# Optimization experiments

Hardware: AMD Instinct MI355X
Metric: run time of the kernel (lower is better)

Reference implementation:

```python
import jax, jax.numpy as jnp
import numpy as np

D_NODE = 256
D_PAIR = 128
C = 32
H = 8
LN_EPS = 1e-5


def layer_norm(x, g, b):
    m = jnp.mean(x, axis=-1, keepdims=True)
    v = jnp.mean(jnp.square(x - m), axis=-1, keepdims=True)
    return (x - m) * jax.lax.rsqrt(v + LN_EPS) * g + b


def self_attention(x, mask, wq, wk, wv, wg, bg, wo, bo=None, bias=None):
    # x: [B, S, R, d], mask: [B, S, R]
    B, S, R, _ = x.shape
    scale = 1.0 / np.sqrt(C)
    q = (jnp.einsum('bsrd,ed->bsre', x, wq) * scale).reshape(B, S, R, H, C)
    k = jnp.einsum('bsrd,ed->bsre', x, wk).reshape(B, S, R, H, C)
    v = jnp.einsum('bsrd,ed->bsre', x, wv).reshape(B, S, R, H, C)
    logits = jnp.einsum('bsqhc,bskhc->bshqk', q, k)
    logits = logits + (1e9 * (mask - 1.0))[:, :, None, None, :]
    if bias is not None:
        logits = logits + bias[:, None]  # [B,1,H,R,R]
    a = jax.nn.softmax(logits, axis=-1)
    o = jnp.einsum('bshqk,bskhc->bsqhc', a, v).reshape(B, S, R, H * C)
    g = jax.nn.sigmoid(jnp.einsum('bsrd,ed->bsre', x, wg) + bg)
    out = jnp.einsum('bsre,de->bsrd', o * g, wo)
    if bo is not None:
        out = out + bo
    return out


def setup_inputs() -> dict:
    key = jax.random.key(0)
    ks = jax.random.split(key, 24)
    B, S, R = 1, 128, 256
    d, dp, hc, dff = D_NODE, D_PAIR, H * C, 4 * D_NODE
    std = 0.02
    inp = {
        'node': jax.random.normal(ks[0], (B, S, R, d), jnp.float32),
        'pair': jax.random.normal(ks[1], (B, R, R, dp), jnp.float32),
        'node_mask': jnp.ones((B, S, R), jnp.float32),
        # row attention (pair-biased)
        'row_ln_m_g': jnp.ones((d,), jnp.float32),
        'row_ln_m_b': jnp.zeros((d,), jnp.float32),
        'row_ln_z_g': jnp.ones((dp,), jnp.float32),
        'row_ln_z_b': jnp.zeros((dp,), jnp.float32),
        'row_b_w': jax.random.normal(ks[2], (H, dp), jnp.float32) / np.sqrt(dp),
        'row_wq': jax.random.normal(ks[3], (hc, d), jnp.float32) * std,
        'row_wk': jax.random.normal(ks[4], (hc, d), jnp.float32) * std,
        'row_wv': jax.random.normal(ks[5], (hc, d), jnp.float32) * std,
        'row_wg': jax.random.normal(ks[6], (hc, d), jnp.float32) * std,
        'row_bg': jnp.ones((hc,), jnp.float32),
        'row_wo': jax.random.normal(ks[7], (d, hc), jnp.float32) * std,
        'row_out_bias': jnp.zeros((d,), jnp.float32),
        # column attention
        'col_ln_g': jnp.ones((d,), jnp.float32),
        'col_ln_b': jnp.zeros((d,), jnp.float32),
        'col_wq': jax.random.normal(ks[8], (hc, d), jnp.float32) * std,
        'col_wk': jax.random.normal(ks[9], (hc, d), jnp.float32) * std,
        'col_wv': jax.random.normal(ks[10], (hc, d), jnp.float32) * std,
        'col_wg': jax.random.normal(ks[11], (hc, d), jnp.float32) * std,
        'col_bg': jnp.ones((hc,), jnp.float32),
        'col_wo': jax.random.normal(ks[12], (d, hc), jnp.float32) * std,
        'col_bo': jnp.zeros((d,), jnp.float32),
        # transition
        'tr_ln_g': jnp.ones((d,), jnp.float32),
        'tr_ln_b': jnp.zeros((d,), jnp.float32),
        'tr_w1': jax.random.normal(ks[13], (dff, d), jnp.float32) * std,
        'tr_b1': jnp.zeros((dff,), jnp.float32),
        'tr_w2': jax.random.normal(ks[14], (d, dff), jnp.float32) * std,
        'tr_b2': jnp.zeros((d,), jnp.float32),
    }
    return inp


def reference(node, pair, node_mask,
              row_ln_m_g, row_ln_m_b, row_ln_z_g, row_ln_z_b, row_b_w,
              row_wq, row_wk, row_wv, row_wg, row_bg, row_wo, row_out_bias,
              col_ln_g, col_ln_b, col_wq, col_wk, col_wv, col_wg, col_bg,
              col_wo, col_bo, tr_ln_g, tr_ln_b, tr_w1, tr_b1, tr_w2, tr_b2):
    # --- MSA row attention with pair bias ---
    M = layer_norm(node, row_ln_m_g, row_ln_m_b)
    Z = layer_norm(pair, row_ln_z_g, row_ln_z_b)
    b = jnp.einsum('bqkd,hd->bhqk', Z, row_b_w)  # pair bias [B,H,R,R]
    attn = self_attention(M, node_mask, row_wq, row_wk, row_wv,
                          row_wg, row_bg, row_wo, bo=None, bias=b)
    # bias_dropout_add in eval mode: residual + attn + fused out bias
    node = node + attn + row_out_bias
    # --- MSA column attention ---
    Mt = jnp.swapaxes(node, 1, 2)            # [B,R,S,d]
    Mn = layer_norm(Mt, col_ln_g, col_ln_b)
    mask_t = jnp.swapaxes(node_mask, 1, 2)   # [B,R,S]
    attn_c = self_attention(Mn, mask_t, col_wq, col_wk, col_wv,
                            col_wg, col_bg, col_wo, bo=col_bo)
    node = node + jnp.swapaxes(attn_c, 1, 2)
    # --- MSA transition ---
    t = layer_norm(node, tr_ln_g, tr_ln_b)
    t = jax.nn.relu(jnp.einsum('bsrd,ed->bsre', t, tr_w1) + tr_b1)
    node = node + (jnp.einsum('bsre,de->bsrd', t, tr_w2) + tr_b2)
    return node
```

## Files before the change

kernel.cpp:

```cpp
#include <hip/hip_runtime.h>
#include <math.h>

#define S 128
#define R 256
#define DMODEL 256
#define H 8
#define CDIM 32
#define HC 256
#define DFF 1024
#define NROWS (S*R)
#define NPAIR (R*R)
#define LN_EPS 1e-5f
#define LOG2E 1.4426950408889634f
#define M32 ((size_t)NROWS * 32)

typedef unsigned short u16;
typedef __attribute__((ext_vector_type(8))) short bf16x8;
typedef __attribute__((ext_vector_type(4))) float f32x4;
typedef __attribute__((ext_vector_type(16))) float f32x16;

__device__ __forceinline__ u16 f2bf(float x) {
  unsigned u = __float_as_uint(x);
  u = (u + 0x7fffu + ((u >> 16) & 1u)) >> 16;
  return (u16)u;
}
__device__ __forceinline__ float bf2f(u16 x) {
  return __uint_as_float(((unsigned)x) << 16);
}
__device__ __forceinline__ unsigned cvt_pk(float a, float b) {
  unsigned r;
  asm("v_cvt_pk_bf16_f32 %0, %1, %2" : "=v"(r) : "v"(a), "v"(b));
  return r;
}
__device__ __forceinline__ void pl32swap(unsigned &a, unsigned &b) {
  asm("v_permlane32_swap_b32 %0, %1" : "+v"(a), "+v"(b));
}
__device__ __forceinline__ bf16x8 mk_frag(unsigned a, unsigned b, unsigned c, unsigned d) {
  uint4 t = make_uint4(a, b, c, d);
  return __builtin_bit_cast(bf16x8, t);
}

__device__ __forceinline__ void gload_lds16(const u16* g, u16* l) {
  __builtin_amdgcn_global_load_lds(
      (const __attribute__((address_space(1))) unsigned int*)g,
      (__attribute__((address_space(3))) unsigned int*)l, 16, 0, 0);
}

struct CvtArgs {
  const float* src[12];
  int off[12];
  int n[12];
  float scale[12];
};

__global__ __launch_bounds__(256) void cvt_w_kernel(CvtArgs a, u16* __restrict__ dst) {
  int sg = blockIdx.y;
  int i = (blockIdx.x * 256 + threadIdx.x) * 4;
  if (i >= a.n[sg]) return;
  float4 v = *(const float4*)(a.src[sg] + i);
  float sc = a.scale[sg];
  uint2 o;
  o.x = cvt_pk(v.x * sc, v.y * sc);
  o.y = cvt_pk(v.z * sc, v.w * sc);
  *(uint2*)(dst + a.off[sg] + i) = o;
}

__global__ __launch_bounds__(256) void ln256_kernel(
    const void* __restrict__ in, u16* __restrict__ out,
    const float* __restrict__ gamma, const float* __restrict__ beta,
    int tmode, int inbf)
{
  int wid = threadIdx.x >> 6, lane = threadIdx.x & 63;
  int m = blockIdx.x * 4 + wid;
  int inrow = m;
  if (tmode) { int r = m >> 7, s = m & 127; inrow = s * R + r; }
  float4 x;
  if (inbf) {
    ushort4 u = *(const ushort4*)((const u16*)in + (size_t)inrow * DMODEL + lane * 4);
    x.x = bf2f(u.x); x.y = bf2f(u.y); x.z = bf2f(u.z); x.w = bf2f(u.w);
  } else {
    x = *(const float4*)((const float*)in + (size_t)inrow * DMODEL + lane * 4);
  }
  float sum = x.x + x.y + x.z + x.w;
  float sq  = x.x*x.x + x.y*x.y + x.z*x.z + x.w*x.w;
  #pragma unroll
  for (int off = 32; off; off >>= 1) {
    sum += __shfl_xor(sum, off);
    sq  += __shfl_xor(sq, off);
  }
  float mean = sum * (1.0f/256.0f);
  float var  = sq  * (1.0f/256.0f) - mean*mean;
  float rstd = rsqrtf(var + LN_EPS);
  float4 g = *(const float4*)(gamma + lane*4);
  float4 b = *(const float4*)(beta  + lane*4);
  uint2 o;
  o.x = cvt_pk((x.x-mean)*rstd*g.x + b.x, (x.y-mean)*rstd*g.y + b.y);
  o.y = cvt_pk((x.z-mean)*rstd*g.z + b.z, (x.w-mean)*rstd*g.w + b.w);
  *(uint2*)(out + (size_t)m * DMODEL + lane*4) = o;
}

__global__ __launch_bounds__(256) void pair_bias_kernel(
    const float* __restrict__ pair, const float* __restrict__ gamma,
    const float* __restrict__ beta, const float* __restrict__ bw,
    u16* __restrict__ bias)
{
  int wid = threadIdx.x >> 6, lane = threadIdx.x & 63;
  int p = blockIdx.x * 4 + wid;
  float2 x = *(const float2*)(pair + (size_t)p * 128 + lane*2);
  float sum = x.x + x.y, sq = x.x*x.x + x.y*x.y;
  #pragma unroll
  for (int off = 32; off; off >>= 1) {
    sum += __shfl_xor(sum, off);
    sq  += __shfl_xor(sq, off);
  }
  float mean = sum * (1.0f/128.0f);
  float rstd = rsqrtf(sq*(1.0f/128.0f) - mean*mean + LN_EPS);
  float z0 = (x.x-mean)*rstd*gamma[lane*2]   + beta[lane*2];
  float z1 = (x.y-mean)*rstd*gamma[lane*2+1] + beta[lane*2+1];
  float a0 = z0*bw[0*128+lane*2] + z1*bw[0*128+lane*2+1];
  float a1 = z0*bw[1*128+lane*2] + z1*bw[1*128+lane*2+1];
  float a2 = z0*bw[2*128+lane*2] + z1*bw[2*128+lane*2+1];
  float a3 = z0*bw[3*128+lane*2] + z1*bw[3*128+lane*2+1];
  float a4 = z0*bw[4*128+lane*2] + z1*bw[4*128+lane*2+1];
  float a5 = z0*bw[5*128+lane*2] + z1*bw[5*128+lane*2+1];
  float a6 = z0*bw[6*128+lane*2] + z1*bw[6*128+lane*2+1];
  float a7 = z0*bw[7*128+lane*2] + z1*bw[7*128+lane*2+1];
  #pragma unroll
  for (int off = 32; off; off >>= 1) {
    a0 += __shfl_xor(a0, off); a1 += __shfl_xor(a1, off);
    a2 += __shfl_xor(a2, off); a3 += __shfl_xor(a3, off);
    a4 += __shfl_xor(a4, off); a5 += __shfl_xor(a5, off);
    a6 += __shfl_xor(a6, off); a7 += __shfl_xor(a7, off);
  }
  float v = a0;
  v = (lane==1)?a1:v; v = (lane==2)?a2:v; v = (lane==3)?a3:v;
  v = (lane==4)?a4:v; v = (lane==5)?a5:v; v = (lane==6)?a6:v; v = (lane==7)?a7:v;
  if (lane < 8) {
    int q = p >> 8, k = p & 255;
    int kt = k >> 5, qt = q >> 5, c31 = q & 31;
    int kk = k & 31;
    int hi2 = (kk >> 2) & 1;
    int j = (kk & 3) | ((kk >> 3) << 2);
    size_t addr = ((((size_t)lane*8 + kt)*8 + qt)*2 + hi2)*512 + (size_t)c31*16 + j;
    bias[addr] = f2bf(v * LOG2E);
  }
}

template<int AM>
__global__ __launch_bounds__(512, 2) void gemm_8ph(
    const u16* __restrict__ A, const u16* __restrict__ W,
    void* __restrict__ Cout, int N, int K,
    int mode, const float* __restrict__ bias, const float* __restrict__ res)
{
  __shared__ u16 lds[2][AM+2][128*32];
  int t = threadIdx.x, lane = t & 63, wv = t >> 6;
  int g16 = (lane >> 4) & 3, l16 = lane & 15;
  int wm = wv >> 2, wn = wv & 3;

  int gx = gridDim.x;
  int nwg = gx * gridDim.y;
  int p = blockIdx.y * gx + blockIdx.x;
  int cpx = nwg >> 3;
  int lg = (p & 7) * cpx + (p >> 3);
  int bn = (lg % gx) * 256;
  int bm = (lg / gx) * (AM * 128);

  int sr = t >> 2;
  int swz8 = ((t & 3) ^ ((sr >> 1) & 3)) << 3;
  int rdch = (g16 ^ ((l16 >> 1) & 3)) << 3;
  int rdoff = l16 * 32 + rdch;
  const int wnh = AM + (wn >> 1);
  const int wnr = (wn & 1) * 2048;

  f32x4 acc[AM*4][4];
  #pragma unroll
  for (int i = 0; i < AM*4; ++i)
    #pragma unroll
    for (int j = 0; j < 4; ++j) acc[i][j] = (f32x4){0.f,0.f,0.f,0.f};

  const int nkt = K >> 5;

#define STAGE(buf_, kc_) do { \
    gload_lds16(A + (size_t)(bm + sr) * K + (kc_) + swz8, &lds[buf_][0][t*8]); \
    if (AM == 2) \
      gload_lds16(A + (size_t)(bm + 128 + sr) * K + (kc_) + swz8, &lds[buf_][1][t*8]); \
    gload_lds16(W + (size_t)(bn + sr) * K + (kc_) + swz8, &lds[buf_][AM][t*8]); \
    gload_lds16(W + (size_t)(bn + 128 + sr) * K + (kc_) + swz8, &lds[buf_][AM+1][t*8]); \
  } while(0)

  STAGE(0, 0);
  for (int kt = 0; kt < nkt; ++kt) {
    if (kt + 1 < nkt) {
      STAGE((kt + 1) & 1, (kt + 1) * 32);
      if (AM == 2) asm volatile("s_waitcnt vmcnt(4)" ::: "memory");
      else         asm volatile("s_waitcnt vmcnt(3)" ::: "memory");
    } else {
      asm volatile("s_waitcnt vmcnt(0)" ::: "memory");
    }
    __builtin_amdgcn_s_barrier();
    int buf = kt & 1;
    const u16* Abase = (AM == 2) ? &lds[buf][wm][0] : &lds[buf][0][wm*2048];
    const u16* Wbase = &lds[buf][wnh][wnr];
    bf16x8 wf[4];
    #pragma unroll
    for (int nf = 0; nf < 4; ++nf)
      wf[nf] = *(const bf16x8*)(Wbase + nf*512 + rdoff);
    __builtin_amdgcn_s_setprio(1);
    #pragma unroll
    for (int mf = 0; mf < AM*4; ++mf) {
      bf16x8 a0 = *(const bf16x8*)(Abase + mf*512 + rdoff);
      #pragma unroll
      for (int nf = 0; nf < 4; ++nf)
        acc[mf][nf] = __builtin_amdgcn_mfma_f32_16x16x32_bf16(wf[nf], a0, acc[mf][nf], 0, 0, 0);
    }
    __builtin_amdgcn_s_setprio(0);
    asm volatile("" ::: "memory");
    __builtin_amdgcn_s_barrier();
  }
#undef STAGE

  const u16* resb = (const u16*)res;
  int rowb = bm + wm*(AM*64) + l16;
  int colb = bn + wn*64 + (g16 << 2);
  #pragma unroll
  for (int mf = 0; mf < AM*4; ++mf) {
    int row = rowb + mf*16;
    #pragma unroll
    for (int nf = 0; nf < 4; ++nf) {
      int col0 = colb + nf*16;
      f32x4 v = acc[mf][nf];
      if (mode == 6) {
        if (col0 >= 768) {
          float4 b4 = *(const float4*)(bias + col0 - 768);
          v[0] = 1.0f/(1.0f+__expf(-(v[0]+b4.x)));
          v[1] = 1.0f/(1.0f+__expf(-(v[1]+b4.y)));
          v[2] = 1.0f/(1.0f+__expf(-(v[2]+b4.z)));
          v[3] = 1.0f/(1.0f+__expf(-(v[3]+b4.w)));
        }
        uint2 o; o.x = cvt_pk(v[0], v[1]); o.y = cvt_pk(v[2], v[3]);
        size_t i2 = (size_t)(col0 >> 5) * M32 + (size_t)row*32 + (col0 & 31);
        *(uint2*)((u16*)Cout + i2) = o;
      } else if (mode == 3) {
        float4 b4 = *(const float4*)(bias + col0);
        uint2 o;
        o.x = cvt_pk(fmaxf(v[0]+b4.x, 0.f), fmaxf(v[1]+b4.y, 0.f));
        o.y = cvt_pk(fmaxf(v[2]+b4.z, 0.f), fmaxf(v[3]+b4.w, 0.f));
        *(uint2*)((u16*)Cout + (size_t)row*N + col0) = o;
      } else if (mode == 4) {
        size_t i2 = (size_t)row*N + col0;
        float4 r4 = *(const float4*)(res + i2);
        float4 b4 = *(const float4*)(bias + col0);
        float4 o = make_float4(v[0]+r4.x+b4.x, v[1]+r4.y+b4.y,
                               v[2]+r4.z+b4.z, v[3]+r4.w+b4.w);
        *(float4*)((float*)Cout + i2) = o;
      } else if (mode == 5) {
        int rr = row >> 7, ss = row & 127;
        size_t i2 = ((size_t)ss*R + rr)*(size_t)N + col0;
        float4 r4 = *(const float4*)(res + i2);
        float4 b4 = *(const float4*)(bias + col0);
        float4 o = make_float4(v[0]+r4.x+b4.x, v[1]+r4.y+b4.y,
                               v[2]+r4.z+b4.z, v[3]+r4.w+b4.w);
        *(float4*)((float*)Cout + i2) = o;
      } else if (mode == 7) {
        size_t i2 = (size_t)row*N + col0;
        float4 r4 = *(const float4*)(res + i2);
        float4 b4 = *(const float4*)(bias + col0);
        uint2 o;
        o.x = cvt_pk(v[0]+r4.x+b4.x, v[1]+r4.y+b4.y);
        o.y = cvt_pk(v[2]+r4.z+b4.z, v[3]+r4.w+b4.w);
        *(uint2*)((u16*)Cout + i2) = o;
      } else if (mode == 8) {
        int rr = row >> 7, ss = row & 127;
        size_t i2 = ((size_t)ss*R + rr)*(size_t)N + col0;
        ushort4 r4 = *(const ushort4*)(resb + i2);
        float4 b4 = *(const float4*)(bias + col0);
        uint2 o;
        o.x = cvt_pk(v[0]+bf2f(r4.x)+b4.x, v[1]+bf2f(r4.y)+b4.y);
        o.y = cvt_pk(v[2]+bf2f(r4.z)+b4.z, v[3]+bf2f(r4.w)+b4.w);
        *(uint2*)((u16*)Cout + i2) = o;
      } else if (mode == 9) {
        size_t i2 = (size_t)row*N + col0;
        ushort4 r4 = *(const ushort4*)(resb + i2);
        float4 b4 = *(const float4*)(bias + col0);
        float4 o = make_float4(v[0]+bf2f(r4.x)+b4.x, v[1]+bf2f(r4.y)+b4.y,
                               v[2]+bf2f(r4.z)+b4.z, v[3]+bf2f(r4.w)+b4.w);
        *(float4*)((float*)Cout + i2) = o;
      } else if (mode == 2) {
        float4 b4 = *(const float4*)(bias + col0);
        uint2 o;
        o.x = cvt_pk(1.0f/(1.0f+__expf(-(v[0]+b4.x))),
                     1.0f/(1.0f+__expf(-(v[1]+b4.y))));
        o.y = cvt_pk(1.0f/(1.0f+__expf(-(v[2]+b4.z))),
                     1.0f/(1.0f+__expf(-(v[3]+b4.w))));
        *(uint2*)((u16*)Cout + (size_t)row*N + col0) = o;
      } else {
        uint2 o; o.x = cvt_pk(v[0], v[1]); o.y = cvt_pk(v[2], v[3]);
        *(uint2*)((u16*)Cout + (size_t)row*N + col0) = o;
      }
    }
  }
}

template<bool RM>
__device__ __forceinline__ void softmax_pack(
    const f32x16 &sac, const float* __restrict__ lmbp,
    bf16x8 bf0, bf16x8 bf1, int kb, int hi,
    float &lsum, bf16x8 &pf0, bf16x8 &pf1)
{
  float p[16];
  #pragma unroll
  for (int rq = 0; rq < 4; ++rq) {
    int k0 = kb + 8*rq + 4*hi;
    float4 lm4 = *(const float4*)&lmbp[k0];
    float b0 = lm4.x, b1 = lm4.y, b2 = lm4.z, b3 = lm4.w;
    if (RM) {
      if (rq < 2) {
        b0 += bf2f((u16)bf0[4*rq+0]); b1 += bf2f((u16)bf0[4*rq+1]);
        b2 += bf2f((u16)bf0[4*rq+2]); b3 += bf2f((u16)bf0[4*rq+3]);
      } else {
        b0 += bf2f((u16)bf1[4*rq-8+0]); b1 += bf2f((u16)bf1[4*rq-8+1]);
        b2 += bf2f((u16)bf1[4*rq-8+2]); b3 += bf2f((u16)bf1[4*rq-8+3]);
      }
    }
    p[4*rq+0] = exp2f(sac[4*rq+0] + b0);
    p[4*rq+1] = exp2f(sac[4*rq+1] + b1);
    p[4*rq+2] = exp2f(sac[4*rq+2] + b2);
    p[4*rq+3] = exp2f(sac[4*rq+3] + b3);
    lsum += (p[4*rq+0] + p[4*rq+1]) + (p[4*rq+2] + p[4*rq+3]);
  }
  unsigned u0 = cvt_pk(p[0],  p[1]),  u1 = cvt_pk(p[2],  p[3]);
  unsigned u2 = cvt_pk(p[4],  p[5]),  u3 = cvt_pk(p[6],  p[7]);
  unsigned u4 = cvt_pk(p[8],  p[9]),  u5 = cvt_pk(p[10], p[11]);
  unsigned u6 = cvt_pk(p[12], p[13]), u7 = cvt_pk(p[14], p[15]);
  pl32swap(u0, u2); pl32swap(u1, u3);
  pl32swap(u4, u6); pl32swap(u5, u7);
  pf0 = mk_frag(u0, u1, u2, u3);
  pf1 = mk_frag(u4, u5, u6, u7);
}

template<int NKEY, int HPB, bool ROWMODE>
__global__ __launch_bounds__(512, 2) void attn_mfma(
    const u16* __restrict__ QKVG, const u16* __restrict__ biasF,
    const float* __restrict__ mask, u16* __restrict__ og)
{
  __shared__ __align__(16) u16 Vt[HPB][32][NKEY + 8];
  __shared__ float lmb[NKEY];
  constexpr int NKV = NKEY / 32;
  constexpr int WPH = 8 / HPB;
  int b = blockIdx.y;
  int t = threadIdx.x, lane = t & 63, w = t >> 6;
  int c31 = lane & 31, hi = lane >> 5;
  int lh = w / WPH, wtile = w % WPH;
  int hh = blockIdx.x * HPB + lh;

  size_t rbase = (size_t)b * NKEY * 32;
  const u16* Qp = QKVG + (size_t)hh * M32 + rbase;
  const u16* Kp = QKVG + (size_t)(8 + hh) * M32 + rbase;
  const u16* Gp = QKVG + (size_t)(24 + hh) * M32 + rbase;

  for (int i = t; i < HPB*NKEY*4; i += 512) {
    int c0 = (i & 3) * 8;
    int key = (i >> 2) & (NKEY - 1);
    int sh = (i >> 2) / NKEY;
    const u16* Vs = QKVG + (size_t)(16 + blockIdx.x*HPB + sh) * M32 + rbase;
    bf16x8 v8 = *(const bf16x8*)(Vs + (size_t)key*32 + c0);
    #pragma unroll
    for (int j = 0; j < 8; ++j) Vt[sh][c0+j][key] = (u16)v8[j];
  }
  for (int i = t; i < NKEY; i += 512)
    lmb[i] = 1.4426950e9f * ((ROWMODE ? mask[b*R + i] : mask[i*R + b]) - 1.0f);
  __syncthreads();

  int qA = wtile*64 + c31, qB = qA + 32;
  int qtA = wtile*2, qtB = wtile*2 + 1;
  bf16x8 qfA0 = *(const bf16x8*)(Qp + (size_t)qA*32 + hi*8);
  bf16x8 qfA1 = *(const bf16x8*)(Qp + (size_t)qA*32 + 16 + hi*8);
  bf16x8 qfB0 = *(const bf16x8*)(Qp + (size_t)qB*32 + hi*8);
  bf16x8 qfB1 = *(const bf16x8*)(Qp + (size_t)qB*32 + 16 + hi*8);

  f32x16 oA = (f32x16)(0.0f), oB = (f32x16)(0.0f);
  float lsA = 0.f, lsB = 0.f;

#define LOADK(d0_, d1_, g_) do { \
    const u16* kr_ = Kp + ((size_t)((g_)*32) + c31)*32 + hi*8; \
    d0_ = *(const bf16x8*)kr_; d1_ = *(const bf16x8*)(kr_ + 16); \
  } while(0)

#define GROUP_BODY(g_, k0_, k1_) do { \
    int kb_ = (g_) * 32; \
    bf16x8 bA0{}, bA1{}, bB0{}, bB1{}; \
    if (ROWMODE) { \
      const u16* bpA_ = biasF + ((((size_t)hh*8 + (g_))*8 + qtA)*2 + hi)*512 + (size_t)c31*16; \
      bA0 = *(const bf16x8*)bpA_; bA1 = *(const bf16x8*)(bpA_ + 8); \
    } \
    __builtin_amdgcn_s_setprio(1); \
    f32x16 sacA_ = __builtin_amdgcn_mfma_f32_32x32x16_bf16(k0_, qfA0, (f32x16)(0.0f), 0, 0, 0); \
    sacA_ = __builtin_amdgcn_mfma_f32_32x32x16_bf16(k1_, qfA1, sacA_, 0, 0, 0); \
    __builtin_amdgcn_s_setprio(0); \
    bf16x8 va0_ = *(const bf16x8*)&Vt[lh][c31][kb_ + hi*8]; \
    bf16x8 va1_ = *(const bf16x8*)&Vt[lh][c31][kb_ + 16 + hi*8]; \
    bf16x8 pf0_, pf1_; \
    softmax_pack<ROWMODE>(sacA_, lmb, bA0, bA1, kb_, hi, lsA, pf0_, pf1_); \
    __builtin_amdgcn_s_setprio(1); \
    oA = __builtin_amdgcn_mfma_f32_32x32x16_bf16(va0_, pf0_, oA, 0, 0, 0); \
    oA = __builtin_amdgcn_mfma_f32_32x32x16_bf16(va1_, pf1_, oA, 0, 0, 0); \
    __builtin_amdgcn_s_setprio(0); \
    if (ROWMODE) { \
      const u16* bpB_ = biasF + ((((size_t)hh*8 + (g_))*8 + qtB)*2 + hi)*512 + (size_t)c31*16; \
      bB0 = *(const bf16x8*)bpB_; bB1 = *(const bf16x8*)(bpB_ + 8); \
    } \
    __builtin_amdgcn_s_setprio(1); \
    f32x16 sacB_ = __builtin_amdgcn_mfma_f32_32x32x16_bf16(k0_, qfB0, (f32x16)(0.0f), 0, 0, 0); \
    sacB_ = __builtin_amdgcn_mfma_f32_32x32x16_bf16(k1_, qfB1, sacB_, 0, 0, 0); \
    __builtin_amdgcn_s_setprio(0); \
    softmax_pack<ROWMODE>(sacB_, lmb, bB0, bB1, kb_, hi, lsB, pf0_, pf1_); \
    __builtin_amdgcn_s_setprio(1); \
    oB = __builtin_amdgcn_mfma_f32_32x32x16_bf16(va0_, pf0_, oB, 0, 0, 0); \
    oB = __builtin_amdgcn_mfma_f32_32x32x16_bf16(va1_, pf1_, oB, 0, 0, 0); \
    __builtin_amdgcn_s_setprio(0); \
  } while(0)

  bf16x8 ke0{}, ke1{}, ko0{}, ko1{};
  LOADK(ke0, ke1, 0);
  LOADK(ko0, ko1, 1);
  for (int g = 0; g < NKV; g += 2) {
    bf16x8 c0 = ke0, c1 = ke1;
    if (g + 2 < NKV) LOADK(ke0, ke1, g + 2);
    GROUP_BODY(g, c0, c1);
    bf16x8 d0 = ko0, d1 = ko1;
    if (g + 3 < NKV) LOADK(ko0, ko1, g + 3);
    GROUP_BODY(g + 1, d0, d1);
  }
#undef GROUP_BODY
#undef LOADK

  lsA += __shfl_xor(lsA, 32);
  lsB += __shfl_xor(lsB, 32);
  float invA = 1.0f / lsA, invB = 1.0f / lsB;

  size_t baseO = (size_t)b * NKEY * 256 + (size_t)hh * 32;
  #pragma unroll
  for (int tile = 0; tile < 2; ++tile) {
    int q = (tile == 0) ? qA : qB;
    float inv = (tile == 0) ? invA : invB;
    const f32x16 &oo = (tile == 0) ? oA : oB;
    u16* op = og + baseO + (size_t)q * 256;
    const u16* gp = Gp + (size_t)q * 32;
    #pragma unroll
    for (int rq = 0; rq < 4; ++rq) {
      int c0 = 8*rq + 4*hi;
      ushort4 g4 = *(const ushort4*)(gp + c0);
      float f0 = oo[4*rq+0] * inv * bf2f(g4.x);
      float f1 = oo[4*rq+1] * inv * bf2f(g4.y);
      float f2 = oo[4*rq+2] * inv * bf2f(g4.z);
      float f3 = oo[4*rq+3] * inv * bf2f(g4.w);
      uint2 o2; o2.x = cvt_pk(f0, f1); o2.y = cvt_pk(f2, f3);
      *(uint2*)(op + c0) = o2;
    }
  }
}

extern "C" void kernel_launch(void* const* d_in, const int* in_sizes, int n_in,
                              void* d_out, int out_size, void* d_ws, size_t ws_size,
                              hipStream_t stream)
{
  const float* node         = (const float*)d_in[0];
  const float* pair         = (const float*)d_in[1];
  const float* node_mask    = (const float*)d_in[2];
  const float* row_ln_m_g   = (const float*)d_in[3];
  const float* row_ln_m_b   = (const float*)d_in[4];
  const float* row_ln_z_g   = (const float*)d_in[5];
  const float* row_ln_z_b   = (const float*)d_in[6];
  const float* row_b_w      = (const float*)d_in[7];
  const float* row_wq       = (const float*)d_in[8];
  const float* row_wk       = (const float*)d_in[9];
  const float* row_wv       = (const float*)d_in[10];
  const float* row_wg       = (const float*)d_in[11];
  const float* row_bg       = (const float*)d_in[12];
  const float* row_wo       = (const float*)d_in[13];
  const float* row_out_bias = (const float*)d_in[14];
  const float* col_ln_g     = (const float*)d_in[15];
  const float* col_ln_b     = (const float*)d_in[16];
  const float* col_wq       = (const float*)d_in[17];
  const float* col_wk       = (const float*)d_in[18];
  const float* col_wv       = (const float*)d_in[19];
  const float* col_wg       = (const float*)d_in[20];
  const float* col_bg       = (const float*)d_in[21];
  const float* col_wo       = (const float*)d_in[22];
  const float* col_bo       = (const float*)d_in[23];
  const float* tr_ln_g      = (const float*)d_in[24];
  const float* tr_ln_b      = (const float*)d_in[25];
  const float* tr_w1        = (const float*)d_in[26];
  const float* tr_b1        = (const float*)d_in[27];
  const float* tr_w2        = (const float*)d_in[28];
  const float* tr_b2        = (const float*)d_in[29];

  float* out = (float*)d_out;
  char* ws8 = (char*)d_ws;
  const size_t MB = 1ull << 20;
  u16*   A     = (u16*)(ws8);
  u16*   QKVG  = (u16*)(ws8 + 16*MB);
  u16*   Ob    = (u16*)(ws8 + 80*MB);
  u16*   DbF   = (u16*)(ws8 + 96*MB);
  u16*   N1    = (u16*)(ws8 + 100*MB);
  u16*   N2    = (u16*)(ws8 + 116*MB);
  u16*   Wb    = (u16*)(ws8 + 132*MB);
  u16*   T1    = QKVG;

  const float qs = 0.17677669529663687f;

  u16* Wrqkvg = Wb + 0;
  u16* Wro    = Wb + 262144;
  u16* Wcqkvg = Wb + 327680;
  u16* Wco    = Wb + 589824;
  u16* W1w    = Wb + 655360;
  u16* W2w    = Wb + 917504;

  CvtArgs ca;
  const float* srcs[12] = {row_wq,row_wk,row_wv,row_wg,row_wo,
                           col_wq,col_wk,col_wv,col_wg,col_wo,tr_w1,tr_w2};
  int offs[12] = {0,65536,131072,196608,262144,327680,393216,458752,524288,589824,655360,917504};
  int ns[12]   = {65536,65536,65536,65536,65536,65536,65536,65536,65536,65536,262144,262144};
  for (int i = 0; i < 12; ++i) {
    ca.src[i] = srcs[i]; ca.off[i] = offs[i]; ca.n[i] = ns[i];
    ca.scale[i] = (i == 0 || i == 5) ? qs * LOG2E : 1.0f;
  }
  cvt_w_kernel<<<dim3(256,12), 256, 0, stream>>>(ca, Wb);

  dim3 gq(4, 128);
  dim3 go(1, 256);

  ln256_kernel<<<8192, 256, 0, stream>>>(node, A, row_ln_m_g, row_ln_m_b, 0, 0);
  pair_bias_kernel<<<16384, 256, 0, stream>>>(pair, row_ln_z_g, row_ln_z_b, row_b_w, DbF);
  gemm_8ph<2><<<gq, 512, 0, stream>>>(A, Wrqkvg, QKVG, 1024, 256, 6, row_bg, nullptr);
  attn_mfma<256,2,true><<<dim3(4,128), 512, 0, stream>>>(QKVG, DbF, node_mask, Ob);
  gemm_8ph<1><<<go, 512, 0, stream>>>(Ob, Wro, N1, 256, 256, 7, row_out_bias, node);

  ln256_kernel<<<8192, 256, 0, stream>>>(N1, A, col_ln_g, col_ln_b, 1, 1);
  gemm_8ph<2><<<gq, 512, 0, stream>>>(A, Wcqkvg, QKVG, 1024, 256, 6, col_bg, nullptr);
  attn_mfma<128,4,false><<<dim3(2,256), 512, 0, stream>>>(QKVG, nullptr, node_mask, Ob);
  gemm_8ph<1><<<go, 512, 0, stream>>>(Ob, Wco, N2, 256, 256, 8, col_bo, (const float*)N1);

  ln256_kernel<<<8192, 256, 0, stream>>>(N2, A, tr_ln_g, tr_ln_b, 0, 1);
  gemm_8ph<2><<<gq, 512, 0, stream>>>(A, W1w, T1, 1024, 256, 3, tr_b1, nullptr);
  gemm_8ph<1><<<go, 512, 0, stream>>>(T1, W2w, out, 256, 1024, 9, tr_b2, (const float*)N2);
}
```

Measured before the change: 352.1 us.

## Add single-shot K=256 GEMM kernel with full-K LDS staging and smaller tiles

Adds a new GEMM kernel for all K=256 projections. It loads the whole 128x256 A and W tiles into LDS in one pass, with no double-buffered K loop, and uses 128x128 output tiles over a larger grid. The old templated kernel is specialised into a K=1024 variant used only for the second transition GEMM, and the epilogue moves into a shared helper. The change removes per-K-step barriers and pipeline overhead and raises the block count, but allows only one block per CU because of 128KB of LDS, and it reloads inputs more often because the tiles are smaller.

Result: no change. 349.9 us (-0.6%).

```diff
diff --git a/kernel.cpp b/kernel.cpp
--- a/kernel.cpp
+++ b/kernel.cpp
@@ -146,13 +146,140 @@
   }
 }
 
-template<int AM>
-__global__ __launch_bounds__(512, 2) void gemm_8ph(
+__device__ __forceinline__ void epi_store(
+    int mode, void* __restrict__ Cout, int N,
+    const float* __restrict__ bias, const float* __restrict__ res,
+    int row, int col0, f32x4 v)
+{
+  const u16* resb = (const u16*)res;
+  if (mode == 6) {
+    if (col0 >= 768) {
+      float4 b4 = *(const float4*)(bias + col0 - 768);
+      v[0] = 1.0f/(1.0f+__expf(-(v[0]+b4.x)));
+      v[1] = 1.0f/(1.0f+__expf(-(v[1]+b4.y)));
+      v[2] = 1.0f/(1.0f+__expf(-(v[2]+b4.z)));
+      v[3] = 1.0f/(1.0f+__expf(-(v[3]+b4.w)));
+    }
+    uint2 o; o.x = cvt_pk(v[0], v[1]); o.y = cvt_pk(v[2], v[3]);
+    size_t i2 = (size_t)(col0 >> 5) * M32 + (size_t)row*32 + (col0 & 31);
+    *(uint2*)((u16*)Cout + i2) = o;
+  } else if (mode == 3) {
+    float4 b4 = *(const float4*)(bias + col0);
+    uint2 o;
+    o.x = cvt_pk(fmaxf(v[0]+b4.x, 0.f), fmaxf(v[1]+b4.y, 0.f));
+    o.y = cvt_pk(fmaxf(v[2]+b4.z, 0.f), fmaxf(v[3]+b4.w, 0.f));
+    *(uint2*)((u16*)Cout + (size_t)row*N + col0) = o;
+  } else if (mode == 7) {
+    size_t i2 = (size_t)row*N + col0;
+    float4 r4 = *(const float4*)(res + i2);
+    float4 b4 = *(const float4*)(bias + col0);
+    uint2 o;
+    o.x = cvt_pk(v[0]+r4.x+b4.x, v[1]+r4.y+b4.y);
+    o.y = cvt_pk(v[2]+r4.z+b4.z, v[3]+r4.w+b4.w);
+    *(uint2*)((u16*)Cout + i2) = o;
+  } else if (mode == 8) {
+    int rr = row >> 7, ss = row & 127;
+    size_t i2 = ((size_t)ss*R + rr)*(size_t)N + col0;
+    ushort4 r4 = *(const ushort4*)(resb + i2);
+    float4 b4 = *(const float4*)(bias + col0);
+    uint2 o;
+    o.x = cvt_pk(v[0]+bf2f(r4.x)+b4.x, v[1]+bf2f(r4.y)+b4.y);
+    o.y = cvt_pk(v[2]+bf2f(r4.z)+b4.z, v[3]+bf2f(r4.w)+b4.w);
+    *(uint2*)((u16*)Cout + i2) = o;
+  } else if (mode == 9) {
+    size_t i2 = (size_t)row*N + col0;
+    ushort4 r4 = *(const ushort4*)(resb + i2);
+    float4 b4 = *(const float4*)(bias + col0);
+    float4 o = make_float4(v[0]+bf2f(r4.x)+b4.x, v[1]+bf2f(r4.y)+b4.y,
+                           v[2]+bf2f(r4.z)+b4.z, v[3]+bf2f(r4.w)+b4.w);
+    *(float4*)((float*)Cout + i2) = o;
+  } else {
+    uint2 o; o.x = cvt_pk(v[0], v[1]); o.y = cvt_pk(v[2], v[3]);
+    *(uint2*)((u16*)Cout + (size_t)row*N + col0) = o;
+  }
+}
+
+__global__ __launch_bounds__(512, 1) void gemm_flat(
+    const u16* __restrict__ A, const u16* __restrict__ W,
+    void* __restrict__ Cout, int N,
+    int mode, const float* __restrict__ bias, const float* __restrict__ res)
+{
+  __shared__ u16 As[128*256];
+  __shared__ u16 Ws[128*256];
+  int t = threadIdx.x, lane = t & 63;
+  int wv = t >> 6;
+  int g16 = (lane >> 4) & 3, l16 = lane & 15;
+  int wm = wv >> 1, wn = wv & 1;
+
+  int gx = gridDim.x;
+  int nwg = gx * gridDim.y;
+  int p = blockIdx.y * gx + blockIdx.x;
+  int cpx = nwg >> 3;
+  int lg = (p & 7) * cpx + (p >> 3);
+  int bn = (lg % gx) * 128;
+  int bm = (lg / gx) * 128;
+
+  int srow = t >> 5;
+  int dc = t & 31;
+  int sc = (dc & 24) | ((dc & 7) ^ (srow & 7));
+  const u16* Ag = A + (size_t)(bm + srow) * 256 + sc * 8;
+  const u16* Wg = W + (size_t)(bn + srow) * 256 + sc * 8;
+  #pragma unroll
+  for (int i = 0; i < 8; ++i)
+    gload_lds16(Ag + (size_t)i * 16 * 256, &As[i*4096 + t*8]);
+  #pragma unroll
+  for (int i = 0; i < 8; ++i)
+    gload_lds16(Wg + (size_t)i * 16 * 256, &Ws[i*4096 + t*8]);
+  asm volatile("s_waitcnt vmcnt(0)" ::: "memory");
+  __builtin_amdgcn_s_barrier();
+
+  f32x4 acc[2][4];
+  #pragma unroll
+  for (int i = 0; i < 2; ++i)
+    #pragma unroll
+    for (int j = 0; j < 4; ++j) acc[i][j] = (f32x4){0.f,0.f,0.f,0.f};
+
+  int swz8 = l16 & 7;
+  const u16* Abase = As + (size_t)(wm*32 + l16) * 256;
+  const u16* Wbase = Ws + (size_t)(wn*64 + l16) * 256;
+
+  #pragma unroll
+  for (int ks = 0; ks < 8; ++ks) {
+    int c0 = ks * 4 + g16;
+    int rdc = (c0 & 24) | ((c0 & 7) ^ swz8);
+    int off = rdc * 8;
+    bf16x8 wf[4];
+    #pragma unroll
+    for (int nf = 0; nf < 4; ++nf)
+      wf[nf] = *(const bf16x8*)(Wbase + nf*16*256 + off);
+    bf16x8 a0 = *(const bf16x8*)(Abase + off);
+    bf16x8 a1 = *(const bf16x8*)(Abase + 16*256 + off);
+    __builtin_amdgcn_s_setprio(1);
+    #pragma unroll
+    for (int nf = 0; nf < 4; ++nf) {
+      acc[0][nf] = __builtin_amdgcn_mfma_f32_16x16x32_bf16(wf[nf], a0, acc[0][nf], 0, 0, 0);
+      acc[1][nf] = __builtin_amdgcn_mfma_f32_16x16x32_bf16(wf[nf], a1, acc[1][nf], 0, 0, 0);
+    }
+    __builtin_amdgcn_s_setprio(0);
+  }
+
+  int rowb = bm + wm*32 + l16;
+  int colb = bn + wn*64 + (g16 << 2);
+  #pragma unroll
+  for (int mf = 0; mf < 2; ++mf) {
+    int row = rowb + mf*16;
+    #pragma unroll
+    for (int nf = 0; nf < 4; ++nf)
+      epi_store(mode, Cout, N, bias, res, row, colb + nf*16, acc[mf][nf]);
+  }
+}
+
+__global__ __launch_bounds__(512, 2) void gemm_k1024(
     const u16* __restrict__ A, const u16* __restrict__ W,
     void* __restrict__ Cout, int N, int K,
     int mode, const float* __restrict__ bias, const float* __restrict__ res)
 {
-  __shared__ u16 lds[2][AM+2][128*32];
+  __shared__ u16 lds[2][3][128*32];
   int t = threadIdx.x, lane = t & 63, wv = t >> 6;
   int g16 = (lane >> 4) & 3, l16 = lane & 15;
   int wm = wv >> 2, wn = wv & 3;
@@ -163,18 +290,18 @@
   int cpx = nwg >> 3;
   int lg = (p & 7) * cpx + (p >> 3);
   int bn = (lg % gx) * 256;
-  int bm = (lg / gx) * (AM * 128);
+  int bm = (lg / gx) * 128;
 
   int sr = t >> 2;
   int swz8 = ((t & 3) ^ ((sr >> 1) & 3)) << 3;
   int rdch = (g16 ^ ((l16 >> 1) & 3)) << 3;
   int rdoff = l16 * 32 + rdch;
-  const int wnh = AM + (wn >> 1);
+  const int wnh = 1 + (wn >> 1);
   const int wnr = (wn & 1) * 2048;
 
-  f32x4 acc[AM*4][4];
-  #pragma unroll
-  for (int i = 0; i < AM*4; ++i)
+  f32x4 acc[4][4];
+  #pragma unroll
+  for (int i = 0; i < 4; ++i)
     #pragma unroll
     for (int j = 0; j < 4; ++j) acc[i][j] = (f32x4){0.f,0.f,0.f,0.f};
 
@@ -182,24 +309,21 @@
 
 #define STAGE(buf_, kc_) do { \
     gload_lds16(A + (size_t)(bm + sr) * K + (kc_) + swz8, &lds[buf_][0][t*8]); \
-    if (AM == 2) \
-      gload_lds16(A + (size_t)(bm + 128 + sr) * K + (kc_) + swz8, &lds[buf_][1][t*8]); \
-    gload_lds16(W + (size_t)(bn + sr) * K + (kc_) + swz8, &lds[buf_][AM][t*8]); \
-    gload_lds16(W + (size_t)(bn + 128 + sr) * K + (kc_) + swz8, &lds[buf_][AM+1][t*8]); \
+    gload_lds16(W + (size_t)(bn + sr) * K + (kc_) + swz8, &lds[buf_][1][t*8]); \
+    gload_lds16(W + (size_t)(bn + 128 + sr) * K + (kc_) + swz8, &lds[buf_][2][t*8]); \
   } while(0)
 
   STAGE(0, 0);
   for (int kt = 0; kt < nkt; ++kt) {
     if (kt + 1 < nkt) {
       STAGE((kt + 1) & 1, (kt + 1) * 32);
-      if (AM == 2) asm volatile("s_waitcnt vmcnt(4)" ::: "memory");
-      else         asm volatile("s_waitcnt vmcnt(3)" ::: "memory");
+      asm volatile("s_waitcnt vmcnt(3)" ::: "memory");
     } else {
       asm volatile("s_waitcnt vmcnt(0)" ::: "memory");
     }
     __builtin_amdgcn_s_barrier();
     int buf = kt & 1;
-    const u16* Abase = (AM == 2) ? &lds[buf][wm][0] : &lds[buf][0][wm*2048];
+    const u16* Abase = &lds[buf][0][wm*2048];
     const u16* Wbase = &lds[buf][wnh][wnr];
     bf16x8 wf[4];
     #pragma unroll
@@ -207,7 +331,7 @@
       wf[nf] = *(const bf16x8*)(Wbase + nf*512 + rdoff);
     __builtin_amdgcn_s_setprio(1);
     #pragma unroll
-    for (int mf = 0; mf < AM*4; ++mf) {
+    for (int mf = 0; mf < 4; ++mf) {
       bf16x8 a0 = *(const bf16x8*)(Abase + mf*512 + rdoff);
       #pragma unroll
       for (int nf = 0; nf < 4; ++nf)
@@ -219,85 +343,14 @@
   }
 #undef STAGE
 
-  const u16* resb = (const u16*)res;
-  int rowb = bm + wm*(AM*64) + l16;
+  int rowb = bm + wm*64 + l16;
   int colb = bn + wn*64 + (g16 << 2);
   #pragma unroll
-  for (int mf = 0; mf < AM*4; ++mf) {
+  for (int mf = 0; mf < 4; ++mf) {
     int row = rowb + mf*16;
     #pragma unroll
-    for (int nf = 0; nf < 4; ++nf) {
-      int col0 = colb + nf*16;
-      f32x4 v = acc[mf][nf];
-      if (mode == 6) {
-        if (col0 >= 768) {
-          float4 b4 = *(const float4*)(bias + col0 - 768);
-          v[0] = 1.0f/(1.0f+__expf(-(v[0]+b4.x)));
-          v[1] = 1.0f/(1.0f+__expf(-(v[1]+b4.y)));
-          v[2] = 1.0f/(1.0f+__expf(-(v[2]+b4.z)));
-          v[3] = 1.0f/(1.0f+__expf(-(v[3]+b4.w)));
-        }
-        uint2 o; o.x = cvt_pk(v[0], v[1]); o.y = cvt_pk(v[2], v[3]);
-        size_t i2 = (size_t)(col0 >> 5) * M32 + (size_t)row*32 + (col0 & 31);
-        *(uint2*)((u16*)Cout + i2) = o;
-      } else if (mode == 3) {
-        float4 b4 = *(const float4*)(bias + col0);
-        uint2 o;
-        o.x = cvt_pk(fmaxf(v[0]+b4.x, 0.f), fmaxf(v[1]+b4.y, 0.f));
-        o.y = cvt_pk(fmaxf(v[2]+b4.z, 0.f), fmaxf(v[3]+b4.w, 0.f));
-        *(uint2*)((u16*)Cout + (size_t)row*N + col0) = o;
-      } else if (mode == 4) {
-        size_t i2 = (size_t)row*N + col0;
-        float4 r4 = *(const float4*)(res + i2);
-        float4 b4 = *(const float4*)(bias + col0);
-        float4 o = make_float4(v[0]+r4.x+b4.x, v[1]+r4.y+b4.y,
-                               v[2]+r4.z+b4.z, v[3]+r4.w+b4.w);
-        *(float4*)((float*)Cout + i2) = o;
-      } else if (mode == 5) {
-        int rr = row >> 7, ss = row & 127;
-        size_t i2 = ((size_t)ss*R + rr)*(size_t)N + col0;
-        float4 r4 = *(const float4*)(res + i2);
-        float4 b4 = *(const float4*)(bias + col0);
-        float4 o = make_float4(v[0]+r4.x+b4.x, v[1]+r4.y+b4.y,
-                               v[2]+r4.z+b4.z, v[3]+r4.w+b4.w);
-        *(float4*)((float*)Cout + i2) = o;
-      } else if (mode == 7) {
-        size_t i2 = (size_t)row*N + col0;
-        float4 r4 = *(const float4*)(res + i2);
-        float4 b4 = *(const float4*)(bias + col0);
-        uint2 o;
-        o.x = cvt_pk(v[0]+r4.x+b4.x, v[1]+r4.y+b4.y);
-        o.y = cvt_pk(v[2]+r4.z+b4.z, v[3]+r4.w+b4.w);
-        *(uint2*)((u16*)Cout + i2) = o;
-      } else if (mode == 8) {
-        int rr = row >> 7, ss = row & 127;
-        size_t i2 = ((size_t)ss*R + rr)*(size_t)N + col0;
-        ushort4 r4 = *(const ushort4*)(resb + i2);
-        float4 b4 = *(const float4*)(bias + col0);
-        uint2 o;
-        o.x = cvt_pk(v[0]+bf2f(r4.x)+b4.x, v[1]+bf2f(r4.y)+b4.y);
-        o.y = cvt_pk(v[2]+bf2f(r4.z)+b4.z, v[3]+bf2f(r4.w)+b4.w);
-        *(uint2*)((u16*)Cout + i2) = o;
-      } else if (mode == 9) {
-        size_t i2 = (size_t)row*N + col0;
-        ushort4 r4 = *(const ushort4*)(resb + i2);
-        float4 b4 = *(const float4*)(bias + col0);
-        float4 o = make_float4(v[0]+bf2f(r4.x)+b4.x, v[1]+bf2f(r4.y)+b4.y,
-                               v[2]+bf2f(r4.z)+b4.z, v[3]+bf2f(r4.w)+b4.w);
-        *(float4*)((float*)Cout + i2) = o;
-      } else if (mode == 2) {
-        float4 b4 = *(const float4*)(bias + col0);
-        uint2 o;
-        o.x = cvt_pk(1.0f/(1.0f+__expf(-(v[0]+b4.x))),
-                     1.0f/(1.0f+__expf(-(v[1]+b4.y))));
-        o.y = cvt_pk(1.0f/(1.0f+__expf(-(v[2]+b4.z))),
-                     1.0f/(1.0f+__expf(-(v[3]+b4.w))));
-        *(uint2*)((u16*)Cout + (size_t)row*N + col0) = o;
-      } else {
-        uint2 o; o.x = cvt_pk(v[0], v[1]); o.y = cvt_pk(v[2], v[3]);
-        *(uint2*)((u16*)Cout + (size_t)row*N + col0) = o;
-      }
-    }
+    for (int nf = 0; nf < 4; ++nf)
+      epi_store(mode, Cout, N, bias, res, row, colb + nf*16, acc[mf][nf]);
   }
 }
 
@@ -527,21 +580,22 @@
   }
   cvt_w_kernel<<<dim3(256,12), 256, 0, stream>>>(ca, Wb);
 
-  dim3 gq(4, 128);
-  dim3 go(1, 256);
+  dim3 gf1024(8, 256);
+  dim3 gf256(2, 256);
+  dim3 gw2(1, 256);
 
   ln256_kernel<<<8192, 256, 0, stream>>>(node, A, row_ln_m_g, row_ln_m_b, 0, 0);
   pair_bias_kernel<<<16384, 256, 0, stream>>>(pair, row_ln_z_g, row_ln_z_b, row_b_w, DbF);
-  gemm_8ph<2><<<gq, 512, 0, stream>>>(A, Wrqkvg, QKVG, 1024, 256, 6, row_bg, nullptr);
+  gemm_flat<<<gf1024, 512, 0, stream>>>(A, Wrqkvg, QKVG, 1024, 6, row_bg, nullptr);
   attn_mfma<256,2,true><<<dim3(4,128), 512, 0, stream>>>(QKVG, DbF, node_mask, Ob);
-  gemm_8ph<1><<<go, 512, 0, stream>>>(Ob, Wro, N1, 256, 256, 7, row_out_bias, node);
+  gemm_flat<<<gf256, 512, 0, stream>>>(Ob, Wro, N1, 256, 7, row_out_bias, node);
 
   ln256_kernel<<<8192, 256, 0, stream>>>(N1, A, col_ln_g, col_ln_b, 1, 1);
-  gemm_8ph<2><<<gq, 512, 0, stream>>>(A, Wcqkvg, QKVG, 1024, 256, 6, col_bg, nullptr);
+  gemm_flat<<<gf1024, 512, 0, stream>>>(A, Wcqkvg, QKVG, 1024, 6, col_bg, nullptr);
   attn_mfma<128,4,false><<<dim3(2,256), 512, 0, stream>>>(QKVG, nullptr, node_mask, Ob);
-  gemm_8ph<1><<<go, 512, 0, stream>>>(Ob, Wco, N2, 256, 256, 8, col_bo, (const float*)N1);
+  gemm_flat<<<gf256, 512, 0, stream>>>(Ob, Wco, N2, 256, 8, col_bo, (const float*)N1);
 
   ln256_kernel<<<8192, 256, 0, stream>>>(N2, A, tr_ln_g, tr_ln_b, 0, 1);
-  gemm_8ph<2><<<gq, 512, 0, stream>>>(A, W1w, T1, 1024, 256, 3, tr_b1, nullptr);
-  gemm_8ph<1><<<go, 512, 0, stream>>>(T1, W2w, out, 256, 1024, 9, tr_b2, (const float*)N2);
-}
+  gemm_flat<<<gf1024, 512, 0, stream>>>(A, W1w, T1, 1024, 3, tr_b1, nullptr);
+  gemm_k1024<<<gw2, 512, 0, stream>>>(T1, W2w, out, 256, 1024, 9, tr_b2, (const float*)N2);
+}
```

## Replace large-tile GEMM with 128x128 tile, 4-wave kernel and more workgroups

Applied to the files above, without the earlier changes.

Replaces the templated 8-wave GEMM (256x256 or 128x256 tiles) with a single 4-wave kernel using 128x128 tiles. Grids grow to 2048 and 512 workgroups, and the epilogue moves into a shared device function with unused modes dropped. The aim is better occupancy and load balance across the GPU's compute units with lower register pressure. The cost is less operand reuse per tile, so each workgroup pulls more global and LDS traffic per FLOP.

After: 313.5 us. 11.0% less time.

```diff
diff --git a/kernel.cpp b/kernel.cpp
--- a/kernel.cpp
+++ b/kernel.cpp
@@ -146,35 +146,85 @@
   }
 }
 
-template<int AM>
-__global__ __launch_bounds__(512, 2) void gemm_8ph(
+__device__ __forceinline__ void epi_store(
+    int mode, void* __restrict__ Cout, int N,
+    const float* __restrict__ bias, const float* __restrict__ res,
+    int row, int col0, f32x4 v)
+{
+  const u16* resb = (const u16*)res;
+  if (mode == 6) {
+    if (col0 >= 768) {
+      float4 b4 = *(const float4*)(bias + col0 - 768);
+      v[0] = 1.0f/(1.0f+__expf(-(v[0]+b4.x)));
+      v[1] = 1.0f/(1.0f+__expf(-(v[1]+b4.y)));
+      v[2] = 1.0f/(1.0f+__expf(-(v[2]+b4.z)));
+      v[3] = 1.0f/(1.0f+__expf(-(v[3]+b4.w)));
+    }
+    uint2 o; o.x = cvt_pk(v[0], v[1]); o.y = cvt_pk(v[2], v[3]);
+    size_t i2 = (size_t)(col0 >> 5) * M32 + (size_t)row*32 + (col0 & 31);
+    *(uint2*)((u16*)Cout + i2) = o;
+  } else if (mode == 3) {
+    float4 b4 = *(const float4*)(bias + col0);
+    uint2 o;
+    o.x = cvt_pk(fmaxf(v[0]+b4.x, 0.f), fmaxf(v[1]+b4.y, 0.f));
+    o.y = cvt_pk(fmaxf(v[2]+b4.z, 0.f), fmaxf(v[3]+b4.w, 0.f));
+    *(uint2*)((u16*)Cout + (size_t)row*N + col0) = o;
+  } else if (mode == 7) {
+    size_t i2 = (size_t)row*N + col0;
+    float4 r4 = *(const float4*)(res + i2);
+    float4 b4 = *(const float4*)(bias + col0);
+    uint2 o;
+    o.x = cvt_pk(v[0]+r4.x+b4.x, v[1]+r4.y+b4.y);
+    o.y = cvt_pk(v[2]+r4.z+b4.z, v[3]+r4.w+b4.w);
+    *(uint2*)((u16*)Cout + i2) = o;
+  } else if (mode == 8) {
+    int rr = row >> 7, ss = row & 127;
+    size_t i2 = ((size_t)ss*R + rr)*(size_t)N + col0;
+    ushort4 r4 = *(const ushort4*)(resb + i2);
+    float4 b4 = *(const float4*)(bias + col0);
+    uint2 o;
+    o.x = cvt_pk(v[0]+bf2f(r4.x)+b4.x, v[1]+bf2f(r4.y)+b4.y);
+    o.y = cvt_pk(v[2]+bf2f(r4.z)+b4.z, v[3]+bf2f(r4.w)+b4.w);
+    *(uint2*)((u16*)Cout + i2) = o;
+  } else if (mode == 9) {
+    size_t i2 = (size_t)row*N + col0;
+    ushort4 r4 = *(const ushort4*)(resb + i2);
+    float4 b4 = *(const float4*)(bias + col0);
+    float4 o = make_float4(v[0]+bf2f(r4.x)+b4.x, v[1]+bf2f(r4.y)+b4.y,
+                           v[2]+bf2f(r4.z)+b4.z, v[3]+bf2f(r4.w)+b4.w);
+    *(float4*)((float*)Cout + i2) = o;
+  } else {
+    uint2 o; o.x = cvt_pk(v[0], v[1]); o.y = cvt_pk(v[2], v[3]);
+    *(uint2*)((u16*)Cout + (size_t)row*N + col0) = o;
+  }
+}
+
+__global__ __launch_bounds__(256, 4) void gemm_v2(
     const u16* __restrict__ A, const u16* __restrict__ W,
     void* __restrict__ Cout, int N, int K,
     int mode, const float* __restrict__ bias, const float* __restrict__ res)
 {
-  __shared__ u16 lds[2][AM+2][128*32];
+  __shared__ u16 lds[2][2][128*32];
   int t = threadIdx.x, lane = t & 63, wv = t >> 6;
   int g16 = (lane >> 4) & 3, l16 = lane & 15;
-  int wm = wv >> 2, wn = wv & 3;
+  int wm = wv >> 1, wn = wv & 1;
 
   int gx = gridDim.x;
   int nwg = gx * gridDim.y;
   int p = blockIdx.y * gx + blockIdx.x;
   int cpx = nwg >> 3;
   int lg = (p & 7) * cpx + (p >> 3);
-  int bn = (lg % gx) * 256;
-  int bm = (lg / gx) * (AM * 128);
+  int bn = (lg % gx) * 128;
+  int bm = (lg / gx) * 128;
 
   int sr = t >> 2;
   int swz8 = ((t & 3) ^ ((sr >> 1) & 3)) << 3;
   int rdch = (g16 ^ ((l16 >> 1) & 3)) << 3;
   int rdoff = l16 * 32 + rdch;
-  const int wnh = AM + (wn >> 1);
-  const int wnr = (wn & 1) * 2048;
-
-  f32x4 acc[AM*4][4];
-  #pragma unroll
-  for (int i = 0; i < AM*4; ++i)
+
+  f32x4 acc[4][4];
+  #pragma unroll
+  for (int i = 0; i < 4; ++i)
     #pragma unroll
     for (int j = 0; j < 4; ++j) acc[i][j] = (f32x4){0.f,0.f,0.f,0.f};
 
@@ -182,32 +232,30 @@
 
 #define STAGE(buf_, kc_) do { \
     gload_lds16(A + (size_t)(bm + sr) * K + (kc_) + swz8, &lds[buf_][0][t*8]); \
-    if (AM == 2) \
-      gload_lds16(A + (size_t)(bm + 128 + sr) * K + (kc_) + swz8, &lds[buf_][1][t*8]); \
-    gload_lds16(W + (size_t)(bn + sr) * K + (kc_) + swz8, &lds[buf_][AM][t*8]); \
-    gload_lds16(W + (size_t)(bn + 128 + sr) * K + (kc_) + swz8, &lds[buf_][AM+1][t*8]); \
+    gload_lds16(A + (size_t)(bm + 64 + sr) * K + (kc_) + swz8, &lds[buf_][0][2048 + t*8]); \
+    gload_lds16(W + (size_t)(bn + sr) * K + (kc_) + swz8, &lds[buf_][1][t*8]); \
+    gload_lds16(W + (size_t)(bn + 64 + sr) * K + (kc_) + swz8, &lds[buf_][1][2048 + t*8]); \
   } while(0)
 
   STAGE(0, 0);
   for (int kt = 0; kt < nkt; ++kt) {
     if (kt + 1 < nkt) {
       STAGE((kt + 1) & 1, (kt + 1) * 32);
-      if (AM == 2) asm volatile("s_waitcnt vmcnt(4)" ::: "memory");
-      else         asm volatile("s_waitcnt vmcnt(3)" ::: "memory");
+      asm volatile("s_waitcnt vmcnt(4)" ::: "memory");
     } else {
       asm volatile("s_waitcnt vmcnt(0)" ::: "memory");
     }
     __builtin_amdgcn_s_barrier();
     int buf = kt & 1;
-    const u16* Abase = (AM == 2) ? &lds[buf][wm][0] : &lds[buf][0][wm*2048];
-    const u16* Wbase = &lds[buf][wnh][wnr];
+    const u16* Abase = &lds[buf][0][wm*2048];
+    const u16* Wbase = &lds[buf][1][wn*2048];
     bf16x8 wf[4];
     #pragma unroll
     for (int nf = 0; nf < 4; ++nf)
       wf[nf] = *(const bf16x8*)(Wbase + nf*512 + rdoff);
     __builtin_amdgcn_s_setprio(1);
     #pragma unroll
-    for (int mf = 0; mf < AM*4; ++mf) {
+    for (int mf = 0; mf < 4; ++mf) {
       bf16x8 a0 = *(const bf16x8*)(Abase + mf*512 + rdoff);
       #pragma unroll
       for (int nf = 0; nf < 4; ++nf)
@@ -219,85 +267,14 @@
   }
 #undef STAGE
 
-  const u16* resb = (const u16*)res;
-  int rowb = bm + wm*(AM*64) + l16;
+  int rowb = bm + wm*64 + l16;
   int colb = bn + wn*64 + (g16 << 2);
   #pragma unroll
-  for (int mf = 0; mf < AM*4; ++mf) {
+  for (int mf = 0; mf < 4; ++mf) {
     int row = rowb + mf*16;
     #pragma unroll
-    for (int nf = 0; nf < 4; ++nf) {
-      int col0 = colb + nf*16;
-      f32x4 v = acc[mf][nf];
-      if (mode == 6) {
-        if (col0 >= 768) {
-          float4 b4 = *(const float4*)(bias + col0 - 768);
-          v[0] = 1.0f/(1.0f+__expf(-(v[0]+b4.x)));
-          v[1] = 1.0f/(1.0f+__expf(-(v[1]+b4.y)));
-          v[2] = 1.0f/(1.0f+__expf(-(v[2]+b4.z)));
-          v[3] = 1.0f/(1.0f+__expf(-(v[3]+b4.w)));
-        }
-        uint2 o; o.x = cvt_pk(v[0], v[1]); o.y = cvt_pk(v[2], v[3]);
-        size_t i2 = (size_t)(col0 >> 5) * M32 + (size_t)row*32 + (col0 & 31);
-        *(uint2*)((u16*)Cout + i2) = o;
-      } else if (mode == 3) {
-        float4 b4 = *(const float4*)(bias + col0);
-        uint2 o;
-        o.x = cvt_pk(fmaxf(v[0]+b4.x, 0.f), fmaxf(v[1]+b4.y, 0.f));
-        o.y = cvt_pk(fmaxf(v[2]+b4.z, 0.f), fmaxf(v[3]+b4.w, 0.f));
-        *(uint2*)((u16*)Cout + (size_t)row*N + col0) = o;
-      } else if (mode == 4) {
-        size_t i2 = (size_t)row*N + col0;
-        float4 r4 = *(const float4*)(res + i2);
-        float4 b4 = *(const float4*)(bias + col0);
-        float4 o = make_float4(v[0]+r4.x+b4.x, v[1]+r4.y+b4.y,
-                               v[2]+r4.z+b4.z, v[3]+r4.w+b4.w);
-        *(float4*)((float*)Cout + i2) = o;
-      } else if (mode == 5) {
-        int rr = row >> 7, ss = row & 127;
-        size_t i2 = ((size_t)ss*R + rr)*(size_t)N + col0;
-        float4 r4 = *(const float4*)(res + i2);
-        float4 b4 = *(const float4*)(bias + col0);
-        float4 o = make_float4(v[0]+r4.x+b4.x, v[1]+r4.y+b4.y,
-                               v[2]+r4.z+b4.z, v[3]+r4.w+b4.w);
-        *(float4*)((float*)Cout + i2) = o;
-      } else if (mode == 7) {
-        size_t i2 = (size_t)row*N + col0;
-        float4 r4 = *(const float4*)(res + i2);
-        float4 b4 = *(const float4*)(bias + col0);
-        uint2 o;
-        o.x = cvt_pk(v[0]+r4.x+b4.x, v[1]+r4.y+b4.y);
-        o.y = cvt_pk(v[2]+r4.z+b4.z, v[3]+r4.w+b4.w);
-        *(uint2*)((u16*)Cout + i2) = o;
-      } else if (mode == 8) {
-        int rr = row >> 7, ss = row & 127;
-        size_t i2 = ((size_t)ss*R + rr)*(size_t)N + col0;
-        ushort4 r4 = *(const ushort4*)(resb + i2);
-        float4 b4 = *(const float4*)(bias + col0);
-        uint2 o;
-        o.x = cvt_pk(v[0]+bf2f(r4.x)+b4.x, v[1]+bf2f(r4.y)+b4.y);
-        o.y = cvt_pk(v[2]+bf2f(r4.z)+b4.z, v[3]+bf2f(r4.w)+b4.w);
-        *(uint2*)((u16*)Cout + i2) = o;
-      } else if (mode == 9) {
-        size_t i2 = (size_t)row*N + col0;
-        ushort4 r4 = *(const ushort4*)(resb + i2);
-        float4 b4 = *(const float4*)(bias + col0);
-        float4 o = make_float4(v[0]+bf2f(r4.x)+b4.x, v[1]+bf2f(r4.y)+b4.y,
-                               v[2]+bf2f(r4.z)+b4.z, v[3]+bf2f(r4.w)+b4.w);
-        *(float4*)((float*)Cout + i2) = o;
-      } else if (mode == 2) {
-        float4 b4 = *(const float4*)(bias + col0);
-        uint2 o;
-        o.x = cvt_pk(1.0f/(1.0f+__expf(-(v[0]+b4.x))),
-                     1.0f/(1.0f+__expf(-(v[1]+b4.y))));
-        o.y = cvt_pk(1.0f/(1.0f+__expf(-(v[2]+b4.z))),
-                     1.0f/(1.0f+__expf(-(v[3]+b4.w))));
-        *(uint2*)((u16*)Cout + (size_t)row*N + col0) = o;
-      } else {
-        uint2 o; o.x = cvt_pk(v[0], v[1]); o.y = cvt_pk(v[2], v[3]);
-        *(uint2*)((u16*)Cout + (size_t)row*N + col0) = o;
-      }
-    }
+    for (int nf = 0; nf < 4; ++nf)
+      epi_store(mode, Cout, N, bias, res, row, colb + nf*16, acc[mf][nf]);
   }
 }
 
@@ -527,21 +504,21 @@
   }
   cvt_w_kernel<<<dim3(256,12), 256, 0, stream>>>(ca, Wb);
 
-  dim3 gq(4, 128);
-  dim3 go(1, 256);
+  dim3 g1024(8, 256);
+  dim3 g256(2, 256);
 
   ln256_kernel<<<8192, 256, 0, stream>>>(node, A, row_ln_m_g, row_ln_m_b, 0, 0);
   pair_bias_kernel<<<16384, 256, 0, stream>>>(pair, row_ln_z_g, row_ln_z_b, row_b_w, DbF);
-  gemm_8ph<2><<<gq, 512, 0, stream>>>(A, Wrqkvg, QKVG, 1024, 256, 6, row_bg, nullptr);
+  gemm_v2<<<g1024, 256, 0, stream>>>(A, Wrqkvg, QKVG, 1024, 256, 6, row_bg, nullptr);
   attn_mfma<256,2,true><<<dim3(4,128), 512, 0, stream>>>(QKVG, DbF, node_mask, Ob);
-  gemm_8ph<1><<<go, 512, 0, stream>>>(Ob, Wro, N1, 256, 256, 7, row_out_bias, node);
+  gemm_v2<<<g256, 256, 0, stream>>>(Ob, Wro, N1, 256, 256, 7, row_out_bias, node);
 
   ln256_kernel<<<8192, 256, 0, stream>>>(N1, A, col_ln_g, col_ln_b, 1, 1);
-  gemm_8ph<2><<<gq, 512, 0, stream>>>(A, Wcqkvg, QKVG, 1024, 256, 6, col_bg, nullptr);
+  gemm_v2<<<g1024, 256, 0, stream>>>(A, Wcqkvg, QKVG, 1024, 256, 6, col_bg, nullptr);
   attn_mfma<128,4,false><<<dim3(2,256), 512, 0, stream>>>(QKVG, nullptr, node_mask, Ob);
-  gemm_8ph<1><<<go, 512, 0, stream>>>(Ob, Wco, N2, 256, 256, 8, col_bo, (const float*)N1);
+  gemm_v2<<<g256, 256, 0, stream>>>(Ob, Wco, N2, 256, 256, 8, col_bo, (const float*)N1);
 
   ln256_kernel<<<8192, 256, 0, stream>>>(N2, A, tr_ln_g, tr_ln_b, 0, 1);
-  gemm_8ph<2><<<gq, 512, 0, stream>>>(A, W1w, T1, 1024, 256, 3, tr_b1, nullptr);
-  gemm_8ph<1><<<go, 512, 0, stream>>>(T1, W2w, out, 256, 1024, 9, tr_b2, (const float*)N2);
-}
+  gemm_v2<<<g1024, 256, 0, stream>>>(A, W1w, T1, 1024, 256, 3, tr_b1, nullptr);
+  gemm_v2<<<g256, 256, 0, stream>>>(T1, W2w, out, 256, 1024, 9, tr_b2, (const float*)N2);
+}
```
